# Kernel optimization log

Hardware: AMD Instinct MI355X
Metric: run time of the kernel (lower is better)

Reference implementation:

```python
import jax, jax.numpy as jnp
import numpy as np

N_NODES = 20000
N_EDGES = 200000
N_SEG = 16      # segments per operand
EXTENT = 32     # uniform segment extent
N_PATHS = 64
OP_SIZE = N_SEG * EXTENT  # 512


def setup_inputs() -> dict:
    key = jax.random.key(0)
    k1, k2, k3, k4, k5, k6 = jax.random.split(key, 6)
    x_nodes = jax.random.normal(k1, (N_NODES, OP_SIZE), dtype=jnp.float32)
    x_edges = jax.random.normal(k2, (N_EDGES, OP_SIZE), dtype=jnp.float32)
    path_coeffs = jax.random.normal(k3, (N_PATHS,), dtype=jnp.float32)
    src = jax.random.randint(k4, (N_EDGES,), 0, N_NODES, dtype=jnp.int64)
    dst = jax.random.randint(k5, (N_EDGES,), 0, N_NODES, dtype=jnp.int64)
    path_indices = jax.random.randint(k6, (N_PATHS, 3), 0, N_SEG, dtype=jnp.int64)
    return {"x_nodes": x_nodes, "x_edges": x_edges, "path_coeffs": path_coeffs,
            "src": src, "dst": dst, "path_indices": path_indices}


def reference(x_nodes, x_edges, path_coeffs, src, dst, path_indices):
    # Segmented polynomial, uniform 1d segments:
    #   for each edge b and path p with segment indices (i1, i2, i3) and coeff c_p:
    #     out[dst[b], i3, :] += c_p * x_nodes[src[b], i1, :] * x_edges[b, i2, :]
    n_nodes = x_nodes.shape[0]
    x1 = x_nodes[src].reshape(-1, N_SEG, EXTENT)        # [M, S, E] gather (input_indices)
    x2 = x_edges.reshape(-1, N_SEG, EXTENT)             # [M, S, E]
    i1, i2, i3 = path_indices[:, 0], path_indices[:, 1], path_indices[:, 2]
    # per-path segmented product with scalar coefficients: [M, P, E]
    contrib = path_coeffs[None, :, None] * x1[:, i1, :] * x2[:, i2, :]
    # segmented accumulation into output segments along axis 1
    edge_out = jnp.zeros((x2.shape[0], N_SEG, EXTENT), x_nodes.dtype).at[:, i3, :].add(contrib)
    # scatter_add edge outputs to nodes (output_indices)
    out = jnp.zeros((n_nodes, OP_SIZE), x_nodes.dtype).at[dst].add(edge_out.reshape(-1, OP_SIZE))
    return out
```

## Files before the change

kernel.cpp:

```cpp
#include <hip/hip_runtime.h>

#define N_NODES  20000
#define N_EDGES  200000
#define N_SEG    16
#define EXTENT   32
#define N_PATHS  64
#define OP_SIZE  (N_SEG * EXTENT)


__global__ void k_hist(const int* __restrict__ dst, int* __restrict__ offsets) {
    int e = blockIdx.x * blockDim.x + threadIdx.x;
    if (e < N_EDGES) atomicAdd(&offsets[dst[e]], 1);
}

__global__ void k_scan(int* __restrict__ offsets) {
    __shared__ int sums[256];
    const int T = 256;
    int tid = threadIdx.x;
    int chunk = (N_NODES + T - 1) / T;
    int lo = tid * chunk;
    int hi = lo + chunk; if (hi > N_NODES) hi = N_NODES;
    int s = 0;
    for (int i = lo; i < hi; ++i) s += offsets[i];
    sums[tid] = s;
    __syncthreads();
    if (tid == 0) {
        int acc = 0;
        for (int i = 0; i < T; ++i) { int v = sums[i]; sums[i] = acc; acc += v; }
    }
    __syncthreads();
    int acc = sums[tid];
    for (int i = lo; i < hi; ++i) { int v = offsets[i]; offsets[i] = acc; acc += v; }
}

__global__ void k_scatter(const int* __restrict__ dst, int* __restrict__ offsets,
                          int* __restrict__ edge_list) {
    int e = blockIdx.x * blockDim.x + threadIdx.x;
    if (e < N_EDGES) {
        int pos = atomicAdd(&offsets[dst[e]], 1);
        edge_list[pos] = e;
    }
}


__global__ __launch_bounds__(256) void k_main(
    const float* __restrict__ x_nodes, const float* __restrict__ x_edges,
    const float* __restrict__ path_coeffs, const int* __restrict__ src,
    const int* __restrict__ path_indices,
    const int* __restrict__ offsets, const int* __restrict__ edge_list,
    float* __restrict__ out)
{
    __shared__ float x1s[OP_SIZE];
    __shared__ float x2s[OP_SIZE];
    __shared__ float p_coef[N_PATHS];
    __shared__ int   p_i1[N_PATHS], p_i2[N_PATHS];
    __shared__ int   p_start[N_SEG + 1];

    const int tid = threadIdx.x;
    const int n   = blockIdx.x;

    if (tid < N_SEG) {
        int cnt = 0;
        for (int p = 0; p < N_PATHS; ++p)
            if (path_indices[p * 3 + 2] == tid) ++cnt;
        p_start[tid + 1] = cnt;
    }
    if (tid == 0) p_start[0] = 0;
    __syncthreads();
    if (tid == 0)
        for (int s = 0; s < N_SEG; ++s) p_start[s + 1] += p_start[s];
    __syncthreads();
    if (tid < N_SEG) {
        int w = p_start[tid];
        for (int p = 0; p < N_PATHS; ++p) {
            if (path_indices[p * 3 + 2] == tid) {
                p_i1[w]   = path_indices[p * 3 + 0];
                p_i2[w]   = path_indices[p * 3 + 1];
                p_coef[w] = path_coeffs[p];
                ++w;
            }
        }
    }
    __syncthreads();

    const int start = (n == 0) ? 0 : offsets[n - 1];
    const int end   = offsets[n];

    const int xl = tid & 31;
    const int s0 = tid >> 5;
    float acc0 = 0.f, acc1 = 0.f;

    for (int ei = start; ei < end; ++ei) {
        const int e  = edge_list[ei];
        const int sn = src[e];
        const float4* x1g = (const float4*)(x_nodes + (size_t)sn * OP_SIZE);
        const float4* x2g = (const float4*)(x_edges + (size_t)e  * OP_SIZE);
        if (tid < 128) ((float4*)x1s)[tid]       = x1g[tid];
        else           ((float4*)x2s)[tid - 128] = x2g[tid - 128];
        __syncthreads();

        {
            float a = 0.f;
            for (int k = p_start[s0]; k < p_start[s0 + 1]; ++k)
                a += p_coef[k] * x1s[p_i1[k] * EXTENT + xl] * x2s[p_i2[k] * EXTENT + xl];
            acc0 += a;
        }
        {
            const int s = s0 + 8;
            float a = 0.f;
            for (int k = p_start[s]; k < p_start[s + 1]; ++k)
                a += p_coef[k] * x1s[p_i1[k] * EXTENT + xl] * x2s[p_i2[k] * EXTENT + xl];
            acc1 += a;
        }
        __syncthreads();
    }

    const size_t ob = (size_t)n * OP_SIZE;
    out[ob + tid]       = acc0;
    out[ob + tid + 256] = acc1;
}


extern "C" void kernel_launch(void* const* d_in, const int* in_sizes, int n_in,
                              void* d_out, int out_size, void* d_ws, size_t ws_size,
                              hipStream_t stream) {
    const float* x_nodes      = (const float*)d_in[0];
    const float* x_edges      = (const float*)d_in[1];
    const float* path_coeffs  = (const float*)d_in[2];
    const int*   src          = (const int*)d_in[3];
    const int*   dst          = (const int*)d_in[4];
    const int*   path_indices = (const int*)d_in[5];
    float* out = (float*)d_out;

    int* offsets   = (int*)d_ws;
    int* edge_list = offsets + N_NODES;

    hipMemsetAsync(d_ws, 0, N_NODES * sizeof(int), stream);
    k_hist   <<<(N_EDGES + 255) / 256, 256, 0, stream>>>(dst, offsets);
    k_scan   <<<1, 256, 0, stream>>>(offsets);
    k_scatter<<<(N_EDGES + 255) / 256, 256, 0, stream>>>(dst, offsets, edge_list);
    k_main   <<<N_NODES, 256, 0, stream>>>(x_nodes, x_edges, path_coeffs, src,
                                           path_indices, offsets, edge_list, out);
}
```

Baseline: 790.9 us.

## Rewrite main kernel as single-wave double-buffered async LDS pipeline with path tables

The main kernel drops from 256-thread blocks to a single 64-lane wave per node. It double-buffers each edge's node and edge rows into LDS with global_load_lds async copies and manual waitcnt, so loading the next edge overlaps compute on the current one and the per-edge block barriers go away. Path metadata is precomputed once by a new kernel. That kernel pairs output segments by count so each half-wave handles one segment of each pair, using packed offset and coefficient records. The scan now runs in LDS with wave shuffles, and the scatter stores (edge, src) pairs so one gather is removed. The cost is fewer threads per node and reliance on hand-written wait counts.

```diff
diff --git a/kernel.cpp b/kernel.cpp
--- a/kernel.cpp
+++ b/kernel.cpp
@@ -1,4 +1,5 @@
 #include <hip/hip_runtime.h>
+#include <stdint.h>
 
 #define N_NODES  20000
 #define N_EDGES  200000
@@ -7,117 +8,179 @@
 #define N_PATHS  64
 #define OP_SIZE  (N_SEG * EXTENT)
 
+#define WAIT_VM0  0x0F70
+#define WAIT_VM4  0x0F74
+
 
 __global__ void k_hist(const int* __restrict__ dst, int* __restrict__ offsets) {
     int e = blockIdx.x * blockDim.x + threadIdx.x;
     if (e < N_EDGES) atomicAdd(&offsets[dst[e]], 1);
 }
 
-__global__ void k_scan(int* __restrict__ offsets) {
-    __shared__ int sums[256];
-    const int T = 256;
-    int tid = threadIdx.x;
-    int chunk = (N_NODES + T - 1) / T;
-    int lo = tid * chunk;
-    int hi = lo + chunk; if (hi > N_NODES) hi = N_NODES;
+__global__ __launch_bounds__(1024) void k_scan(int* __restrict__ offsets) {
+    __shared__ int buf[N_NODES];
+    __shared__ int wsum[16];
+    const int tid = threadIdx.x;
+    for (int i = tid; i < N_NODES; i += 1024) buf[i] = offsets[i];
+    __syncthreads();
+    const int C = (N_NODES + 1023) / 1024;
+    int lo = tid * C;
+    int hi = lo + C; if (hi > N_NODES) hi = N_NODES; if (lo > N_NODES) lo = N_NODES;
     int s = 0;
-    for (int i = lo; i < hi; ++i) s += offsets[i];
-    sums[tid] = s;
-    __syncthreads();
-    if (tid == 0) {
-        int acc = 0;
-        for (int i = 0; i < T; ++i) { int v = sums[i]; sums[i] = acc; acc += v; }
-    }
-    __syncthreads();
-    int acc = sums[tid];
-    for (int i = lo; i < hi; ++i) { int v = offsets[i]; offsets[i] = acc; acc += v; }
-}
-
-__global__ void k_scatter(const int* __restrict__ dst, int* __restrict__ offsets,
-                          int* __restrict__ edge_list) {
+    for (int i = lo; i < hi; ++i) s += buf[i];
+    const int lane = tid & 63, w = tid >> 6;
+    int v = s;
+    for (int d = 1; d < 64; d <<= 1) { int t = __shfl_up(v, d); if (lane >= d) v += t; }
+    if (lane == 63) wsum[w] = v;
+    __syncthreads();
+    int wpre = 0;
+    for (int q = 0; q < w; ++q) wpre += wsum[q];
+    int acc = wpre + v - s;
+    for (int i = lo; i < hi; ++i) { int t = buf[i]; buf[i] = acc; acc += t; }
+    __syncthreads();
+    for (int i = tid; i < N_NODES; i += 1024) offsets[i] = buf[i];
+}
+
+__global__ void k_scatter(const int* __restrict__ dst, const int* __restrict__ src,
+                          int* __restrict__ offsets, int2* __restrict__ el2) {
     int e = blockIdx.x * blockDim.x + threadIdx.x;
     if (e < N_EDGES) {
         int pos = atomicAdd(&offsets[dst[e]], 1);
-        edge_list[pos] = e;
+        el2[pos] = make_int2(e, src[e]);
     }
 }
 
-
-__global__ __launch_bounds__(256) void k_main(
+__global__ void k_paths(const int* __restrict__ pi, const float* __restrict__ pc,
+                        int* __restrict__ ks2g, int4* __restrict__ rec2,
+                        int* __restrict__ segmap) {
+    __shared__ int   s_i1[N_PATHS], s_i2[N_PATHS], s_i3[N_PATHS];
+    __shared__ float s_c[N_PATHS];
+    __shared__ int4  s_rec[N_PATHS];
+    __shared__ int   s_total;
+    const int p = threadIdx.x;
+    s_i1[p] = pi[3 * p]; s_i2[p] = pi[3 * p + 1]; s_i3[p] = pi[3 * p + 2];
+    s_c[p]  = pc[p];
+    __syncthreads();
+    if (p == 0) {
+        int cnt[N_SEG];
+        for (int s = 0; s < N_SEG; ++s) cnt[s] = 0;
+        for (int q = 0; q < N_PATHS; ++q) cnt[s_i3[q]]++;
+        int order[N_SEG];
+        for (int s = 0; s < N_SEG; ++s) order[s] = s;
+        for (int a = 1; a < N_SEG; ++a) {
+            int o = order[a], b = a;
+            while (b > 0 && cnt[order[b - 1]] < cnt[o]) { order[b] = order[b - 1]; --b; }
+            order[b] = o;
+        }
+        int ks[9]; ks[0] = 0;
+        for (int t = 0; t < 8; ++t) {
+            int slo = order[2 * t], shi = order[2 * t + 1];
+            segmap[t] = slo; segmap[8 + t] = shi;
+            int L = cnt[slo] > cnt[shi] ? cnt[slo] : cnt[shi];
+            int wlo = ks[t], whi = ks[t];
+            for (int r = 0; r < L; ++r) { int4 z = {0, 0, 0, 0}; s_rec[ks[t] + r] = z; }
+            for (int q = 0; q < N_PATHS; ++q) {
+                if (s_i3[q] == slo) {
+                    s_rec[wlo].x = ((s_i1[q] * EXTENT) << 16) | (s_i2[q] * EXTENT);
+                    s_rec[wlo].y = __float_as_int(s_c[q]); ++wlo;
+                }
+                if (s_i3[q] == shi) {
+                    s_rec[whi].z = ((s_i1[q] * EXTENT) << 16) | (s_i2[q] * EXTENT);
+                    s_rec[whi].w = __float_as_int(s_c[q]); ++whi;
+                }
+            }
+            ks[t + 1] = ks[t] + L;
+        }
+        for (int t = 0; t < 9; ++t) ks2g[t] = ks[t];
+        s_total = ks[8];
+    }
+    __syncthreads();
+    if (p < s_total) rec2[p] = s_rec[p];
+}
+
+
+__device__ __forceinline__ void async16(const float* g, float* l) {
+    __builtin_amdgcn_global_load_lds(
+        (const __attribute__((address_space(1))) uint32_t*)g,
+        (__attribute__((address_space(3))) uint32_t*)l, 16, 0, 0);
+}
+
+__device__ __forceinline__ void stage(const float* __restrict__ x_nodes,
+                                      const float* __restrict__ x_edges,
+                                      int2 m, float* l, int lane) {
+    const float* gn = x_nodes + (size_t)m.y * OP_SIZE + lane * 4;
+    const float* ge = x_edges + (size_t)m.x * OP_SIZE + lane * 4;
+    async16(gn,       l);
+    async16(gn + 256, l + 256);
+    async16(ge,       l + 512);
+    async16(ge + 256, l + 768);
+}
+
+__global__ __launch_bounds__(64, 5) void k_main(
     const float* __restrict__ x_nodes, const float* __restrict__ x_edges,
-    const float* __restrict__ path_coeffs, const int* __restrict__ src,
-    const int* __restrict__ path_indices,
-    const int* __restrict__ offsets, const int* __restrict__ edge_list,
-    float* __restrict__ out)
+    const int* __restrict__ offsets, const int2* __restrict__ el2,
+    const int* __restrict__ ks2g, const int4* __restrict__ rec2,
+    const int* __restrict__ segmap, float* __restrict__ out)
 {
-    __shared__ float x1s[OP_SIZE];
-    __shared__ float x2s[OP_SIZE];
-    __shared__ float p_coef[N_PATHS];
-    __shared__ int   p_i1[N_PATHS], p_i2[N_PATHS];
-    __shared__ int   p_start[N_SEG + 1];
-
-    const int tid = threadIdx.x;
-    const int n   = blockIdx.x;
-
-    if (tid < N_SEG) {
-        int cnt = 0;
-        for (int p = 0; p < N_PATHS; ++p)
-            if (path_indices[p * 3 + 2] == tid) ++cnt;
-        p_start[tid + 1] = cnt;
-    }
-    if (tid == 0) p_start[0] = 0;
-    __syncthreads();
-    if (tid == 0)
-        for (int s = 0; s < N_SEG; ++s) p_start[s + 1] += p_start[s];
-    __syncthreads();
-    if (tid < N_SEG) {
-        int w = p_start[tid];
-        for (int p = 0; p < N_PATHS; ++p) {
-            if (path_indices[p * 3 + 2] == tid) {
-                p_i1[w]   = path_indices[p * 3 + 0];
-                p_i2[w]   = path_indices[p * 3 + 1];
-                p_coef[w] = path_coeffs[p];
-                ++w;
-            }
-        }
-    }
-    __syncthreads();
+    __shared__ float lds[2 * 1024];
+
+    const int lane = threadIdx.x;
+    const int xl   = lane & 31;
+    const int h    = lane >> 5;
+    const int n    = blockIdx.x;
+
+    int ks2[9];
+#pragma unroll
+    for (int j = 0; j < 9; ++j) ks2[j] = ks2g[j];
+    int myseg[8];
+#pragma unroll
+    for (int j = 0; j < 8; ++j) myseg[j] = segmap[h * 8 + j];
 
     const int start = (n == 0) ? 0 : offsets[n - 1];
     const int end   = offsets[n];
-
-    const int xl = tid & 31;
-    const int s0 = tid >> 5;
-    float acc0 = 0.f, acc1 = 0.f;
-
-    for (int ei = start; ei < end; ++ei) {
-        const int e  = edge_list[ei];
-        const int sn = src[e];
-        const float4* x1g = (const float4*)(x_nodes + (size_t)sn * OP_SIZE);
-        const float4* x2g = (const float4*)(x_edges + (size_t)e  * OP_SIZE);
-        if (tid < 128) ((float4*)x1s)[tid]       = x1g[tid];
-        else           ((float4*)x2s)[tid - 128] = x2g[tid - 128];
-        __syncthreads();
-
-        {
-            float a = 0.f;
-            for (int k = p_start[s0]; k < p_start[s0 + 1]; ++k)
-                a += p_coef[k] * x1s[p_i1[k] * EXTENT + xl] * x2s[p_i2[k] * EXTENT + xl];
-            acc0 += a;
-        }
-        {
-            const int s = s0 + 8;
-            float a = 0.f;
-            for (int k = p_start[s]; k < p_start[s + 1]; ++k)
-                a += p_coef[k] * x1s[p_i1[k] * EXTENT + xl] * x2s[p_i2[k] * EXTENT + xl];
-            acc1 += a;
-        }
-        __syncthreads();
+    const int deg   = end - start;
+
+    float acc[8];
+#pragma unroll
+    for (int j = 0; j < 8; ++j) acc[j] = 0.f;
+
+    int2 mq = make_int2(0, 0);
+    if (deg > 0) stage(x_nodes, x_edges, el2[start],     lds,        lane);
+    if (deg > 1) stage(x_nodes, x_edges, el2[start + 1], lds + 1024, lane);
+    if (deg > 2) mq = el2[start + 2];
+
+    for (int i = 0; i < deg; ++i) {
+        int2 mf = make_int2(0, 0);
+        if (i + 3 < deg) mf = el2[start + i + 3];
+
+        if (i + 1 < deg) __builtin_amdgcn_s_waitcnt(WAIT_VM4);
+        else             __builtin_amdgcn_s_waitcnt(WAIT_VM0);
+        __builtin_amdgcn_sched_barrier(0);
+
+        const float* b1 = lds + ((i & 1) << 10);
+        const float* b2 = b1 + 512;
+#pragma unroll
+        for (int j = 0; j < 8; ++j) {
+            float a = acc[j];
+            for (int k = ks2[j]; k < ks2[j + 1]; ++k) {
+                int4 r = rec2[k];
+                int   off = h ? r.z : r.x;
+                float cf  = __int_as_float(h ? r.w : r.y);
+                a = fmaf(cf, b1[(off >> 16) + xl] * b2[(off & 0xffff) + xl], a);
+            }
+            acc[j] = a;
+        }
+
+        if (i + 2 < deg) {
+            stage(x_nodes, x_edges, mq, lds + ((i & 1) << 10), lane);
+            mq = mf;
+        }
     }
 
-    const size_t ob = (size_t)n * OP_SIZE;
-    out[ob + tid]       = acc0;
-    out[ob + tid + 256] = acc1;
+    float* row = out + (size_t)n * OP_SIZE;
+#pragma unroll
+    for (int j = 0; j < 8; ++j)
+        row[myseg[j] * EXTENT + xl] = acc[j];
 }
 
 
@@ -132,13 +195,18 @@
     const int*   path_indices = (const int*)d_in[5];
     float* out = (float*)d_out;
 
-    int* offsets   = (int*)d_ws;
-    int* edge_list = offsets + N_NODES;
-
-    hipMemsetAsync(d_ws, 0, N_NODES * sizeof(int), stream);
+    char* ws = (char*)d_ws;
+    int*  offsets = (int*)ws;                          ws += N_NODES * sizeof(int);
+    int2* el2     = (int2*)ws;                         ws += N_EDGES * sizeof(int2);
+    int4* rec2    = (int4*)ws;                         ws += N_PATHS * sizeof(int4);
+    int*  ks2g    = (int*)ws;                          ws += 16 * sizeof(int);
+    int*  segmap  = (int*)ws;
+
+    hipMemsetAsync(offsets, 0, N_NODES * sizeof(int), stream);
     k_hist   <<<(N_EDGES + 255) / 256, 256, 0, stream>>>(dst, offsets);
-    k_scan   <<<1, 256, 0, stream>>>(offsets);
-    k_scatter<<<(N_EDGES + 255) / 256, 256, 0, stream>>>(dst, offsets, edge_list);
-    k_main   <<<N_NODES, 256, 0, stream>>>(x_nodes, x_edges, path_coeffs, src,
-                                           path_indices, offsets, edge_list, out);
-}
+    k_scan   <<<1, 1024, 0, stream>>>(offsets);
+    k_scatter<<<(N_EDGES + 255) / 256, 256, 0, stream>>>(dst, src, offsets, el2);
+    k_paths  <<<1, 64, 0, stream>>>(path_indices, path_coeffs, ks2g, rec2, segmap);
+    k_main   <<<N_NODES, 64, 0, stream>>>(x_nodes, x_edges, offsets, el2,
+                                          ks2g, rec2, segmap, out);
+}
```

Result: faster. 725.6 us (-8.2%).
